# Kernel tuning notes

Hardware: AMD Instinct MI355X
Metric: run time of the kernel (lower is better)

Reference implementation:

```python
import jax, jax.numpy as jnp
import numpy as np

B, N, D = 32, 2048, 512

def setup_inputs() -> dict:
    key = jax.random.key(0)
    k1, k2, k3, k4 = jax.random.split(key, 4)
    return {
        "src": jax.random.normal(k1, (B, N, 3), dtype=jnp.float32),
        "tgt": jax.random.normal(k2, (B, N, 3), dtype=jnp.float32),
        "src_embed": jax.random.normal(k3, (B, N, D), dtype=jnp.float32),
        "tgt_embed": jax.random.normal(k4, (B, N, D), dtype=jnp.float32),
    }

def reference(src, tgt, src_embed, tgt_embed):
    # src, tgt: (B, N, 3); src_embed, tgt_embed: (B, N, D)
    d_k = jnp.asarray(src_embed.shape[-1], dtype=src_embed.dtype)
    # attention scores (B, N_src, N_tgt), softmax over tgt points
    scores = jnp.einsum('bnd,bmd->bnm', src_embed, tgt_embed) / jnp.sqrt(d_k)
    pointer = jax.nn.softmax(scores, axis=2)
    # matched = tgt^T @ pointer^T -> (B, 3, N_src)
    matched = jnp.einsum('bmc,bnm->bcn', tgt, pointer)
    src_t = jnp.transpose(src, (0, 2, 1))  # (B, 3, N)
    src_cent = jnp.mean(src_t, axis=2, keepdims=True)        # (B, 3, 1)
    matched_cent = jnp.mean(matched, axis=2, keepdims=True)  # (B, 3, 1)
    src_demean = src_t - src_cent
    matched_demean = matched - matched_cent
    # cross-covariance H: (B, 3, 3)
    H = jnp.einsum('bcn,bdn->bcd', src_demean, matched_demean)
    U, _, Vh = jnp.linalg.svd(H, full_matrices=False)  # square 3x3: reduced == full
    V = jnp.transpose(Vh, (0, 2, 1))
    R = jnp.matmul(V, jnp.transpose(U, (0, 2, 1)))
    det = jnp.linalg.det(R)
    identity = jnp.eye(3, dtype=R.dtype)
    reflect = jnp.diag(jnp.array([1.0, 1.0, -1.0], dtype=R.dtype))
    refl = jnp.where((det >= 0)[:, None, None], identity, reflect)
    R = jnp.matmul(refl, R)
    t = jnp.matmul(-R, src_cent) + matched_cent  # (B, 3, 1)
    t = jnp.transpose(t, (0, 2, 1))              # (B, 1, 3)
    return (R, t)
```

## Files before the change

### kernel.cpp

```cpp
#include <hip/hip_runtime.h>
#include <hip/hip_fp16.h>
#include <math.h>

#define B_ 32
#define N_ 2048
#define D_ 512
#define NT 256

typedef __attribute__((ext_vector_type(8))) _Float16 f16x8;
typedef __attribute__((ext_vector_type(8))) short s16x8;
typedef __attribute__((ext_vector_type(4))) float f32x4;
typedef __attribute__((ext_vector_type(16))) float f32x16;
typedef __attribute__((ext_vector_type(4))) unsigned int u32x4;

__device__ inline unsigned packh2(float lo, float hi) {
    __half l = __float2half_rn(lo), h = __float2half_rn(hi);
    return (unsigned)__half_as_ushort(l) | ((unsigned)__half_as_ushort(h) << 16);
}
__device__ inline unsigned f2bf(float x) {
    unsigned u = __float_as_uint(x);
    return (u + 0x7FFFu + ((u >> 16) & 1u)) >> 16;
}
__device__ inline float bf2f(unsigned h) { return __uint_as_float(h << 16); }

__global__ __launch_bounds__(256) void prepass_kernel(
    const float* __restrict__ te, u32x4* __restrict__ kp)
{
    const int idx = blockIdx.x * 256 + threadIdx.x;
    const int b   = idx >> 17;
    const int r17 = idx & 131071;
    const int mt  = r17 >> 13;
    const int kt  = (r17 >> 9) & 15;
    const int o16 = r17 & 511;
    const int r   = o16 >> 2;
    const int s   = o16 & 3;
    const int lg  = s ^ ((r >> 1) & 3);
    const float* src = te + (((size_t)b * N_ + mt * 128 + r) * D_ + kt * 32 + lg * 8);
    const float4 f0 = *(const float4*)src;
    const float4 f1 = *(const float4*)(src + 4);
    u32x4 u;
    u[0] = packh2(f0.x, f0.y);
    u[1] = packh2(f0.z, f0.w);
    u[2] = packh2(f1.x, f1.y);
    u[3] = packh2(f1.z, f1.w);
    kp[idx] = u;
}

__global__ __launch_bounds__(NT, 2) void attn_db32_kernel(
    const float* __restrict__ src, const float* __restrict__ tgt,
    const float* __restrict__ src_embed, const u32x4* __restrict__ kp,
    float* __restrict__ partials)
{
    __shared__ f16x8 Kbuf[2][4][512];
    __shared__ float4 TsB[2][128];
    __shared__ double red[4][15];

    const int tid  = threadIdx.x;
    const int wv   = tid >> 6;
    const int lane = tid & 63;
    const int lr   = lane & 31;
    const int hi   = lane >> 5;
    char* KbufB = (char*)&Kbuf[0][0][0];

    const int sw   = (lr >> 1) & 3;
    const int sxb0 = ((0 + hi) ^ sw) << 4;
    const int sxb1 = ((2 + hi) ^ sw) << 4;

    const int xcd  = blockIdx.x & 7;
    const int idx  = blockIdx.x >> 3;
    const int b    = xcd * 4 + (idx >> 4);
    const int msl  = idx & 15;
    const int n0   = msl * 128;
    const int pblk = b * 16 + msl;

    const float QSC = 0.044194173824159216f * 1.4426950408889634f;
    const int qrow = n0 + wv * 32 + lr;
    f16x8 Qr[32];
    {
        const float* qp = src_embed + ((size_t)b * N_ + qrow) * D_ + hi * 8;
#pragma unroll
        for (int s = 0; s < 32; ++s) {
            const float4 f0 = *(const float4*)(qp + s * 16);
            const float4 f1 = *(const float4*)(qp + s * 16 + 4);
            u32x4 u;
            u[0] = packh2(f0.x * QSC, f0.y * QSC);
            u[1] = packh2(f0.z * QSC, f0.w * QSC);
            u[2] = packh2(f1.x * QSC, f1.y * QSC);
            u[3] = packh2(f1.z * QSC, f1.w * QSC);
            Qr[s] = __builtin_bit_cast(f16x8, u);
        }
    }
    if (tid < 128) {
        const float* tp = tgt + ((size_t)b * N_ + tid) * 3;
        TsB[0][tid] = make_float4(tp[0], tp[1], tp[2], 0.f);
    }

#define STAGE_TILE(t_, half_, ti_) do {                                        \
    const u32x4* _g = kp +                                                     \
        ((((size_t)b * 16 + ((t_) >> 4)) * 16 + ((t_) & 15)) << 9);            \
    __builtin_amdgcn_global_load_lds(                                          \
        (const __attribute__((address_space(1))) void*)(_g + tid),             \
        (__attribute__((address_space(3))) void*)(&Kbuf[half_][ti_][wv * 64]), \
        16, 0, 0);                                                             \
    __builtin_amdgcn_global_load_lds(                                          \
        (const __attribute__((address_space(1))) void*)(_g + 256 + tid),       \
        (__attribute__((address_space(3))) void*)(&Kbuf[half_][ti_][256 + wv * 64]),\
        16, 0, 0);                                                             \
} while (0)

#define STAGE_GROUP(gi_, half_) do {                                           \
    STAGE_TILE(4 * (gi_) + 0, half_, 0);                                       \
    STAGE_TILE(4 * (gi_) + 1, half_, 1);                                       \
    STAGE_TILE(4 * (gi_) + 2, half_, 2);                                       \
    STAGE_TILE(4 * (gi_) + 3, half_, 3);                                       \
} while (0)

    STAGE_GROUP(0, 0);

    float m_s = -1e30f, l_s = 0.f, axs = 0.f, ays = 0.f, azs = 0.f;
    f32x16 acc[4];

    for (int g4 = 0; g4 < 16; ++g4) {
#pragma unroll
        for (int gm = 0; gm < 4; ++gm) {
            const int g = (g4 << 2) | gm;
            __syncthreads();
            if (g < 63) {
                const int gn = g + 1;
                STAGE_GROUP(gn, gn & 1);
            }
            float tv0 = 0.f, tv1 = 0.f, tv2 = 0.f;
            const bool pf = (gm == 3) && (g4 < 15) && (tid < 128);
            if (pf) {
                const float* tp = tgt + ((size_t)b * N_ + (g4 + 1) * 128 + tid) * 3;
                tv0 = tp[0]; tv1 = tp[1]; tv2 = tp[2];
            }
            if (gm == 0) {
#pragma unroll
                for (int rg = 0; rg < 4; ++rg)
#pragma unroll
                    for (int r16 = 0; r16 < 16; ++r16) acc[rg][r16] = 0.f;
            }
            const char* gbase = KbufB + ((g & 1) << 15) + lr * 64;
            __builtin_amdgcn_s_setprio(1);
#pragma unroll
            for (int ti = 0; ti < 4; ++ti) {
                const char* tb = gbase + (ti << 13);
#pragma unroll
                for (int kh = 0; kh < 2; ++kh) {
                    const int sxb = kh ? sxb1 : sxb0;
                    const f16x8 q = Qr[(((gm << 2) | ti) << 1) | kh];
#pragma unroll
                    for (int rg = 0; rg < 4; ++rg) {
                        const f16x8 a = *(const f16x8*)(tb + rg * 2048 + sxb);
                        acc[rg] = __builtin_amdgcn_mfma_f32_32x32x16_f16(
                            a, q, acc[rg], 0, 0, 0);
                    }
                }
            }
            __builtin_amdgcn_s_setprio(0);
            if (pf)
                TsB[(g4 + 1) & 1][tid] = make_float4(tv0, tv1, tv2, 0.f);

            if (gm == 3) {
                const float4* Ts = &TsB[g4 & 1][0];
                float mx = -1e30f;
#pragma unroll
                for (int rg = 0; rg < 4; ++rg)
#pragma unroll
                    for (int r16 = 0; r16 < 16; ++r16)
                        mx = fmaxf(mx, acc[rg][r16]);
                mx = fmaxf(mx, __shfl_xor(mx, 32));
                const float mn = fmaxf(m_s, mx);
                const float c  = exp2f(m_s - mn);
                l_s *= c; axs *= c; ays *= c; azs *= c; m_s = mn;
                float l0 = 0.f, x0 = 0.f, y0 = 0.f, z0 = 0.f;
#pragma unroll
                for (int rg = 0; rg < 4; ++rg)
#pragma unroll
                    for (int r16 = 0; r16 < 16; ++r16) {
                        const int kr = (r16 & 3) + 8 * (r16 >> 2) + 4 * hi + 32 * rg;
                        const float4 tv = Ts[kr];
                        const float p = exp2f(acc[rg][r16] - mn);
                        l0 += p;
                        x0 = fmaf(p, tv.x, x0);
                        y0 = fmaf(p, tv.y, y0);
                        z0 = fmaf(p, tv.z, z0);
                    }
                l_s += l0; axs += x0; ays += y0; azs += z0;
            }
        }
    }
#undef STAGE_GROUP
#undef STAGE_TILE

    l_s += __shfl_xor(l_s, 32);
    axs += __shfl_xor(axs, 32);
    ays += __shfl_xor(ays, 32);
    azs += __shfl_xor(azs, 32);

    double dl[15];
#pragma unroll
    for (int i = 0; i < 15; ++i) dl[i] = 0.0;
    if (hi == 0) {
        const float* sp = src + ((size_t)b * N_ + qrow) * 3;
        const double inv = 1.0 / (double)l_s;
        const double m0d = (double)axs * inv;
        const double m1d = (double)ays * inv;
        const double m2d = (double)azs * inv;
        const double s0 = sp[0], s1 = sp[1], s2 = sp[2];
        dl[0] = s0;  dl[1] = s1;  dl[2] = s2;
        dl[3] = m0d; dl[4] = m1d; dl[5] = m2d;
        dl[6]  = s0 * m0d; dl[7]  = s0 * m1d; dl[8]  = s0 * m2d;
        dl[9]  = s1 * m0d; dl[10] = s1 * m1d; dl[11] = s1 * m2d;
        dl[12] = s2 * m0d; dl[13] = s2 * m1d; dl[14] = s2 * m2d;
    }
#pragma unroll
    for (int i = 0; i < 15; ++i) {
        double v = dl[i];
        for (int off = 1; off < 64; off <<= 1) v += __shfl_xor(v, off);
        dl[i] = v;
    }
    if (lane == 0) {
#pragma unroll
        for (int i = 0; i < 15; ++i) red[wv][i] = dl[i];
    }
    __syncthreads();
    if (tid < 15) {
        double sum = 0.0;
        for (int w = 0; w < 4; ++w) sum += red[w][tid];
        partials[(size_t)pblk * 15 + tid] = (float)sum;
    }
}

__global__ __launch_bounds__(256, 2) void attn_v2_kernel(
    const float* __restrict__ src, const float* __restrict__ tgt,
    const float* __restrict__ src_embed, const float* __restrict__ tgt_embed,
    float* __restrict__ partials)
{
    __shared__ short Khi_s[128 * 64];
    __shared__ short Klo_s[128 * 64];
    __shared__ float4 Ts4[128];
    __shared__ double red[64][15];

    char* KhiB = (char*)Khi_s;
    char* KloB = (char*)Klo_s;

    const int w    = blockIdx.x;
    const int xcd  = w & 7;
    const int idx  = w >> 3;
    const int b    = xcd * 4 + (idx >> 5);
    const int n0   = (idx & 31) * 64;
    const int blk  = b * 32 + (idx & 31);

    const int tid  = threadIdx.x;
    const int wv   = tid >> 6;
    const int lane = tid & 63;
    const int lr   = lane & 15;
    const int lg   = lane >> 4;
    const unsigned swl = (unsigned)((lr & 7) << 4);

    const float scale = 0.044194173824159216f;
    const float* kbase = tgt_embed + (size_t)b * N_ * D_;

    const int qrow = n0 + wv * 16 + lr;
    const float* qp = src_embed + ((size_t)b * N_ + qrow) * D_ + lg * 8;
    s16x8 qhi[16], qlo[16];
#pragma unroll
    for (int s = 0; s < 16; ++s) {
        const float4 f0 = *reinterpret_cast<const float4*>(qp + s * 32);
        const float4 f1 = *reinterpret_cast<const float4*>(qp + s * 32 + 4);
        const float x[8] = {f0.x, f0.y, f0.z, f0.w, f1.x, f1.y, f1.z, f1.w};
#pragma unroll
        for (int i = 0; i < 8; ++i) {
            const float v = x[i] * scale;
            const unsigned h = f2bf(v);
            qhi[s][i] = (short)h;
            qlo[s][i] = (short)f2bf(v - bf2f(h));
        }
    }

    float m_run = -1e30f, l_run = 0.f, a0 = 0.f, a1 = 0.f, a2 = 0.f;
    const int srow = tid >> 1;
    const int shalf = tid & 1;
    const unsigned swr = (unsigned)((srow & 7) << 4);

    for (int m0 = 0; m0 < N_; m0 += 128) {
        f32x4 acc[8];
#pragma unroll
        for (int nf = 0; nf < 8; ++nf) acc[nf] = (f32x4){0.f, 0.f, 0.f, 0.f};

#pragma unroll
        for (int kt = 0; kt < 8; ++kt) {
            __syncthreads();
            {
                const float* gp = kbase + (size_t)(m0 + srow) * D_ + kt * 64 + shalf * 32;
#pragma unroll
                for (int grp = 0; grp < 4; ++grp) {
                    const float4 fa = *reinterpret_cast<const float4*>(gp + grp * 8);
                    const float4 fb = *reinterpret_cast<const float4*>(gp + grp * 8 + 4);
                    const float x[8] = {fa.x, fa.y, fa.z, fa.w, fb.x, fb.y, fb.z, fb.w};
                    s16x8 hi, lo;
#pragma unroll
                    for (int i = 0; i < 8; ++i) {
                        const unsigned h = f2bf(x[i]);
                        hi[i] = (short)h;
                        lo[i] = (short)f2bf(x[i] - bf2f(h));
                    }
                    const unsigned off = (unsigned)srow * 128u +
                        (((unsigned)(shalf * 64 + grp * 16)) ^ swr);
                    *reinterpret_cast<s16x8*>(KhiB + off) = hi;
                    *reinterpret_cast<s16x8*>(KloB + off) = lo;
                }
                if (kt == 0 && tid < 128) {
                    const float* tp = tgt + ((size_t)b * N_ + m0 + tid) * 3;
                    Ts4[tid] = make_float4(tp[0], tp[1], tp[2], 0.f);
                }
            }
            __syncthreads();
#pragma unroll
            for (int ks = 0; ks < 2; ++ks) {
                const int s = kt * 2 + ks;
                const unsigned kb = ((unsigned)(lg * 16 + ks * 64)) ^ swl;
#pragma unroll
                for (int nf = 0; nf < 8; ++nf) {
                    const unsigned off = (unsigned)(nf * 16 + lr) * 128u + kb;
                    const s16x8 ah = *reinterpret_cast<const s16x8*>(KhiB + off);
                    const s16x8 al = *reinterpret_cast<const s16x8*>(KloB + off);
                    acc[nf] = __builtin_amdgcn_mfma_f32_16x16x32_bf16(ah, qhi[s], acc[nf], 0, 0, 0);
                    acc[nf] = __builtin_amdgcn_mfma_f32_16x16x32_bf16(al, qhi[s], acc[nf], 0, 0, 0);
                    acc[nf] = __builtin_amdgcn_mfma_f32_16x16x32_bf16(ah, qlo[s], acc[nf], 0, 0, 0);
                }
            }
        }

        float mx = -1e30f;
#pragma unroll
        for (int nf = 0; nf < 8; ++nf)
#pragma unroll
            for (int r = 0; r < 4; ++r) mx = fmaxf(mx, acc[nf][r]);
        mx = fmaxf(mx, __shfl_xor(mx, 16));
        mx = fmaxf(mx, __shfl_xor(mx, 32));

        const float mnew = fmaxf(m_run, mx);
        const float corr = __expf(m_run - mnew);
        l_run *= corr; a0 *= corr; a1 *= corr; a2 *= corr;

        float ps = 0.f, p0 = 0.f, p1 = 0.f, p2 = 0.f;
#pragma unroll
        for (int nf = 0; nf < 8; ++nf)
#pragma unroll
            for (int r = 0; r < 4; ++r) {
                const float p = __expf(acc[nf][r] - mnew);
                const int n = nf * 16 + lg * 4 + r;
                const float4 tv = Ts4[n];
                ps += p;
                p0 = fmaf(p, tv.x, p0);
                p1 = fmaf(p, tv.y, p1);
                p2 = fmaf(p, tv.z, p2);
            }
        l_run += ps; a0 += p0; a1 += p1; a2 += p2;
        m_run = mnew;
    }

    l_run += __shfl_xor(l_run, 16); l_run += __shfl_xor(l_run, 32);
    a0 += __shfl_xor(a0, 16); a0 += __shfl_xor(a0, 32);
    a1 += __shfl_xor(a1, 16); a1 += __shfl_xor(a1, 32);
    a2 += __shfl_xor(a2, 16); a2 += __shfl_xor(a2, 32);

    __syncthreads();
    if (lg == 0) {
        const float inv = 1.0f / l_run;
        const double mx0 = (double)(a0 * inv);
        const double mx1 = (double)(a1 * inv);
        const double mx2 = (double)(a2 * inv);
        const float* sp = src + ((size_t)b * N_ + qrow) * 3;
        const double s0 = sp[0], s1 = sp[1], s2 = sp[2];
        double* rp = red[wv * 16 + lr];
        rp[0] = s0;  rp[1] = s1;  rp[2] = s2;
        rp[3] = mx0; rp[4] = mx1; rp[5] = mx2;
        rp[6]  = s0 * mx0; rp[7]  = s0 * mx1; rp[8]  = s0 * mx2;
        rp[9]  = s1 * mx0; rp[10] = s1 * mx1; rp[11] = s1 * mx2;
        rp[12] = s2 * mx0; rp[13] = s2 * mx1; rp[14] = s2 * mx2;
    }
    __syncthreads();
    if (tid < 15) {
        double sum = 0.0;
        for (int j = 0; j < 64; ++j) sum += red[j][tid];
        partials[(size_t)blk * 15 + tid] = (float)sum;
    }
}

__global__ void kabsch_kernel(const float* __restrict__ partials,
                              float* __restrict__ out, int nbb)
{
    const int b = threadIdx.x;
    if (b >= B_) return;

    double acc[15];
#pragma unroll
    for (int i = 0; i < 15; ++i) acc[i] = 0.0;
    for (int rb = 0; rb < nbb; ++rb) {
        const float* p = partials + ((size_t)b * nbb + rb) * 15;
#pragma unroll
        for (int i = 0; i < 15; ++i) acc[i] += (double)p[i];
    }

    const double invN = 1.0 / (double)N_;
    const double S[3] = {acc[0], acc[1], acc[2]};
    const double M[3] = {acc[3], acc[4], acc[5]};
    double H[3][3];
    for (int c = 0; c < 3; ++c)
        for (int d = 0; d < 3; ++d)
            H[c][d] = acc[6 + c * 3 + d] - S[c] * M[d] * invN;

    double A[3][3];
    for (int i = 0; i < 3; ++i)
        for (int j = 0; j < 3; ++j)
            A[i][j] = H[0][i] * H[0][j] + H[1][i] * H[1][j] + H[2][i] * H[2][j];

    double V[3][3] = {{1, 0, 0}, {0, 1, 0}, {0, 0, 1}};
    const int PQ[3][2] = {{0, 1}, {0, 2}, {1, 2}};
    for (int sweep = 0; sweep < 20; ++sweep) {
        const double off = fabs(A[0][1]) + fabs(A[0][2]) + fabs(A[1][2]);
        if (off < 1e-24) break;
        for (int pi = 0; pi < 3; ++pi) {
            const int p = PQ[pi][0], q = PQ[pi][1], rr = 3 - p - q;
            const double apq = A[p][q];
            if (fabs(apq) < 1e-300) continue;
            const double theta = (A[q][q] - A[p][p]) / (2.0 * apq);
            const double tt = (theta >= 0.0 ? 1.0 : -1.0) /
                              (fabs(theta) + sqrt(1.0 + theta * theta));
            const double c = 1.0 / sqrt(1.0 + tt * tt);
            const double sn = tt * c;
            const double app = A[p][p], aqq = A[q][q];
            const double arp = A[rr][p], arq = A[rr][q];
            A[p][p] = app - tt * apq;
            A[q][q] = aqq + tt * apq;
            A[p][q] = A[q][p] = 0.0;
            A[rr][p] = A[p][rr] = c * arp - sn * arq;
            A[rr][q] = A[q][rr] = sn * arp + c * arq;
            for (int k = 0; k < 3; ++k) {
                const double vkp = V[k][p], vkq = V[k][q];
                V[k][p] = c * vkp - sn * vkq;
                V[k][q] = sn * vkp + c * vkq;
            }
        }
    }

    double R[3][3] = {{0, 0, 0}, {0, 0, 0}, {0, 0, 0}};
    for (int i = 0; i < 3; ++i) {
        const double lam = A[i][i];
        const double sig = sqrt(lam > 0.0 ? lam : 0.0);
        const double inv = 1.0 / (sig > 1e-30 ? sig : 1e-30);
        double wv[3];
        for (int c = 0; c < 3; ++c)
            wv[c] = H[c][0] * V[0][i] + H[c][1] * V[1][i] + H[c][2] * V[2][i];
        for (int r = 0; r < 3; ++r)
            for (int c = 0; c < 3; ++c)
                R[r][c] += V[r][i] * wv[c] * inv;
    }

    const double det =
        R[0][0] * (R[1][1] * R[2][2] - R[1][2] * R[2][1]) -
        R[0][1] * (R[1][0] * R[2][2] - R[1][2] * R[2][0]) +
        R[0][2] * (R[1][0] * R[2][1] - R[1][1] * R[2][0]);
    if (det < 0.0) {
        R[2][0] = -R[2][0]; R[2][1] = -R[2][1]; R[2][2] = -R[2][2];
    }

    double t[3];
    for (int c = 0; c < 3; ++c)
        t[c] = M[c] * invN -
               (R[c][0] * S[0] + R[c][1] * S[1] + R[c][2] * S[2]) * invN;

    for (int r = 0; r < 3; ++r)
        for (int c = 0; c < 3; ++c)
            out[(size_t)b * 9 + r * 3 + c] = (float)R[r][c];
    for (int c = 0; c < 3; ++c)
        out[(size_t)B_ * 9 + (size_t)b * 3 + c] = (float)t[c];
}

extern "C" void kernel_launch(void* const* d_in, const int* in_sizes, int n_in,
                              void* d_out, int out_size, void* d_ws, size_t ws_size,
                              hipStream_t stream) {
    const float* src = (const float*)d_in[0];
    const float* tgt = (const float*)d_in[1];
    const float* se  = (const float*)d_in[2];
    const float* te  = (const float*)d_in[3];
    float* out = (float*)d_out;

    const size_t KP_OFF = 32768;
    const size_t need = KP_OFF + (size_t)B_ * N_ * D_ * 2;

    if (ws_size >= need) {
        u32x4* kp = (u32x4*)((char*)d_ws + KP_OFF);
        prepass_kernel<<<dim3(16384), dim3(256), 0, stream>>>(te, kp);
        attn_db32_kernel<<<dim3(512), dim3(NT), 0, stream>>>(
            src, tgt, se, kp, (float*)d_ws);
        kabsch_kernel<<<dim3(1), dim3(64), 0, stream>>>((float*)d_ws, out, 16);
    } else {
        attn_v2_kernel<<<dim3(1024), dim3(256), 0, stream>>>(
            src, tgt, se, te, (float*)d_ws);
        kabsch_kernel<<<dim3(1), dim3(64), 0, stream>>>((float*)d_ws, out, 32);
    }
}
```

Before: 233.6 us.

## Use 16x16x32 MFMA with 8 waves per block to cut registers

The attention kernel now runs 8 waves of 16 query rows each, instead of 4 waves of 32 rows. It switches from the 32x32x16 to the 16x16x32 f16 MFMA, which halves the per-lane Q fragment and accumulator register footprint. Launch bounds now ask for 4 blocks per CU rather than 2, so more waves are resident to hide LDS and MFMA latency. In exchange each K tile fragment read from LDS is reused across fewer query rows, so LDS read traffic per FLOP doubles, and the softmax reduction needs an extra cross-lane shuffle.

```diff
diff --git a/kernel.cpp b/kernel.cpp
--- a/kernel.cpp
+++ b/kernel.cpp
@@ -5,12 +5,11 @@
 #define B_ 32
 #define N_ 2048
 #define D_ 512
-#define NT 256
+#define NT 512
 
 typedef __attribute__((ext_vector_type(8))) _Float16 f16x8;
 typedef __attribute__((ext_vector_type(8))) short s16x8;
 typedef __attribute__((ext_vector_type(4))) float f32x4;
-typedef __attribute__((ext_vector_type(16))) float f32x16;
 typedef __attribute__((ext_vector_type(4))) unsigned int u32x4;
 
 __device__ inline unsigned packh2(float lo, float hi) {
@@ -46,25 +45,22 @@
     kp[idx] = u;
 }
 
-__global__ __launch_bounds__(NT, 2) void attn_db32_kernel(
+__global__ __launch_bounds__(NT, 4) void attn_hw_kernel(
     const float* __restrict__ src, const float* __restrict__ tgt,
     const float* __restrict__ src_embed, const u32x4* __restrict__ kp,
     float* __restrict__ partials)
 {
     __shared__ f16x8 Kbuf[2][4][512];
     __shared__ float4 TsB[2][128];
-    __shared__ double red[4][15];
+    __shared__ double red[8][15];
 
     const int tid  = threadIdx.x;
     const int wv   = tid >> 6;
     const int lane = tid & 63;
-    const int lr   = lane & 31;
-    const int hi   = lane >> 5;
+    const int lr   = lane & 15;
+    const int lg   = lane >> 4;
+    const int sxb  = (lg ^ ((lr >> 1) & 3)) << 4;
     char* KbufB = (char*)&Kbuf[0][0][0];
-
-    const int sw   = (lr >> 1) & 3;
-    const int sxb0 = ((0 + hi) ^ sw) << 4;
-    const int sxb1 = ((2 + hi) ^ sw) << 4;
 
     const int xcd  = blockIdx.x & 7;
     const int idx  = blockIdx.x >> 3;
@@ -74,14 +70,14 @@
     const int pblk = b * 16 + msl;
 
     const float QSC = 0.044194173824159216f * 1.4426950408889634f;
-    const int qrow = n0 + wv * 32 + lr;
-    f16x8 Qr[32];
+    const int qrow = n0 + wv * 16 + lr;
+    f16x8 Qr[16];
     {
-        const float* qp = src_embed + ((size_t)b * N_ + qrow) * D_ + hi * 8;
-#pragma unroll
-        for (int s = 0; s < 32; ++s) {
-            const float4 f0 = *(const float4*)(qp + s * 16);
-            const float4 f1 = *(const float4*)(qp + s * 16 + 4);
+        const float* qp = src_embed + ((size_t)b * N_ + qrow) * D_ + lg * 8;
+#pragma unroll
+        for (int s = 0; s < 16; ++s) {
+            const float4 f0 = *(const float4*)(qp + s * 32);
+            const float4 f1 = *(const float4*)(qp + s * 32 + 4);
             u32x4 u;
             u[0] = packh2(f0.x * QSC, f0.y * QSC);
             u[1] = packh2(f0.z * QSC, f0.w * QSC);
@@ -102,10 +98,6 @@
         (const __attribute__((address_space(1))) void*)(_g + tid),             \
         (__attribute__((address_space(3))) void*)(&Kbuf[half_][ti_][wv * 64]), \
         16, 0, 0);                                                             \
-    __builtin_amdgcn_global_load_lds(                                          \
-        (const __attribute__((address_space(1))) void*)(_g + 256 + tid),       \
-        (__attribute__((address_space(3))) void*)(&Kbuf[half_][ti_][256 + wv * 64]),\
-        16, 0, 0);                                                             \
 } while (0)
 
 #define STAGE_GROUP(gi_, half_) do {                                           \
@@ -118,7 +110,7 @@
     STAGE_GROUP(0, 0);
 
     float m_s = -1e30f, l_s = 0.f, axs = 0.f, ays = 0.f, azs = 0.f;
-    f32x16 acc[4];
+    f32x4 acc[8];
 
     for (int g4 = 0; g4 < 16; ++g4) {
 #pragma unroll
@@ -137,25 +129,20 @@
             }
             if (gm == 0) {
 #pragma unroll
-                for (int rg = 0; rg < 4; ++rg)
-#pragma unroll
-                    for (int r16 = 0; r16 < 16; ++r16) acc[rg][r16] = 0.f;
-            }
-            const char* gbase = KbufB + ((g & 1) << 15) + lr * 64;
+                for (int nf = 0; nf < 8; ++nf)
+                    acc[nf] = (f32x4){0.f, 0.f, 0.f, 0.f};
+            }
+            const char* gbase = KbufB + ((g & 1) << 15) + lr * 64 + sxb;
             __builtin_amdgcn_s_setprio(1);
 #pragma unroll
             for (int ti = 0; ti < 4; ++ti) {
+                const int kt = (gm << 2) | ti;
                 const char* tb = gbase + (ti << 13);
 #pragma unroll
-                for (int kh = 0; kh < 2; ++kh) {
-                    const int sxb = kh ? sxb1 : sxb0;
-                    const f16x8 q = Qr[(((gm << 2) | ti) << 1) | kh];
-#pragma unroll
-                    for (int rg = 0; rg < 4; ++rg) {
-                        const f16x8 a = *(const f16x8*)(tb + rg * 2048 + sxb);
-                        acc[rg] = __builtin_amdgcn_mfma_f32_32x32x16_f16(
-                            a, q, acc[rg], 0, 0, 0);
-                    }
+                for (int nf = 0; nf < 8; ++nf) {
+                    const f16x8 a = *(const f16x8*)(tb + nf * 1024);
+                    acc[nf] = __builtin_amdgcn_mfma_f32_16x16x32_f16(
+                        a, Qr[kt], acc[nf], 0, 0, 0);
                 }
             }
             __builtin_amdgcn_s_setprio(0);
@@ -166,22 +153,22 @@
                 const float4* Ts = &TsB[g4 & 1][0];
                 float mx = -1e30f;
 #pragma unroll
-                for (int rg = 0; rg < 4; ++rg)
-#pragma unroll
-                    for (int r16 = 0; r16 < 16; ++r16)
-                        mx = fmaxf(mx, acc[rg][r16]);
+                for (int nf = 0; nf < 8; ++nf)
+#pragma unroll
+                    for (int r4 = 0; r4 < 4; ++r4)
+                        mx = fmaxf(mx, acc[nf][r4]);
+                mx = fmaxf(mx, __shfl_xor(mx, 16));
                 mx = fmaxf(mx, __shfl_xor(mx, 32));
                 const float mn = fmaxf(m_s, mx);
                 const float c  = exp2f(m_s - mn);
                 l_s *= c; axs *= c; ays *= c; azs *= c; m_s = mn;
                 float l0 = 0.f, x0 = 0.f, y0 = 0.f, z0 = 0.f;
 #pragma unroll
-                for (int rg = 0; rg < 4; ++rg)
-#pragma unroll
-                    for (int r16 = 0; r16 < 16; ++r16) {
-                        const int kr = (r16 & 3) + 8 * (r16 >> 2) + 4 * hi + 32 * rg;
-                        const float4 tv = Ts[kr];
-                        const float p = exp2f(acc[rg][r16] - mn);
+                for (int nf = 0; nf < 8; ++nf)
+#pragma unroll
+                    for (int r4 = 0; r4 < 4; ++r4) {
+                        const float4 tv = Ts[nf * 16 + lg * 4 + r4];
+                        const float p = exp2f(acc[nf][r4] - mn);
                         l0 += p;
                         x0 = fmaf(p, tv.x, x0);
                         y0 = fmaf(p, tv.y, y0);
@@ -194,15 +181,15 @@
 #undef STAGE_GROUP
 #undef STAGE_TILE
 
-    l_s += __shfl_xor(l_s, 32);
-    axs += __shfl_xor(axs, 32);
-    ays += __shfl_xor(ays, 32);
-    azs += __shfl_xor(azs, 32);
+    l_s += __shfl_xor(l_s, 16); l_s += __shfl_xor(l_s, 32);
+    axs += __shfl_xor(axs, 16); axs += __shfl_xor(axs, 32);
+    ays += __shfl_xor(ays, 16); ays += __shfl_xor(ays, 32);
+    azs += __shfl_xor(azs, 16); azs += __shfl_xor(azs, 32);
 
     double dl[15];
 #pragma unroll
     for (int i = 0; i < 15; ++i) dl[i] = 0.0;
-    if (hi == 0) {
+    if (lg == 0) {
         const float* sp = src + ((size_t)b * N_ + qrow) * 3;
         const double inv = 1.0 / (double)l_s;
         const double m0d = (double)axs * inv;
@@ -228,7 +215,7 @@
     __syncthreads();
     if (tid < 15) {
         double sum = 0.0;
-        for (int w = 0; w < 4; ++w) sum += red[w][tid];
+        for (int w = 0; w < 8; ++w) sum += red[w][tid];
         partials[(size_t)pblk * 15 + tid] = (float)sum;
     }
 }
@@ -496,7 +483,7 @@
     if (ws_size >= need) {
         u32x4* kp = (u32x4*)((char*)d_ws + KP_OFF);
         prepass_kernel<<<dim3(16384), dim3(256), 0, stream>>>(te, kp);
-        attn_db32_kernel<<<dim3(512), dim3(NT), 0, stream>>>(
+        attn_hw_kernel<<<dim3(512), dim3(NT), 0, stream>>>(
             src, tgt, se, kp, (float*)d_ws);
         kabsch_kernel<<<dim3(1), dim3(64), 0, stream>>>((float*)d_ws, out, 16);
     } else {
```

After: 255.7 us. 1.09x slower.
